# Kernel optimization log

Measured on AMD Instinct MI355X. Metric: run time of the kernel, lower is better.

Reference implementation:

```python
import jax, jax.numpy as jnp
import numpy as np

B, C, L = 4, 256, 4096
C8 = C // 8


def setup_inputs() -> dict:
    key = jax.random.key(0)
    ks = jax.random.split(key, 7)
    s = 0.05
    return {
        "x": jax.random.normal(ks[0], (B, C, L), dtype=jnp.float32),
        "Wq": jax.random.normal(ks[1], (C8, C), dtype=jnp.float32) * s,
        "bq": jax.random.normal(ks[2], (C8,), dtype=jnp.float32) * s,
        "Wk": jax.random.normal(ks[3], (C8, C), dtype=jnp.float32) * s,
        "bk": jax.random.normal(ks[4], (C8,), dtype=jnp.float32) * s,
        "Wv": jax.random.normal(ks[5], (C, C), dtype=jnp.float32) * s,
        "bv": jax.random.normal(ks[6], (C,), dtype=jnp.float32) * s,
        "gamma": jnp.zeros((1,), dtype=jnp.float32),
    }


def reference(x, Wq, bq, Wk, bk, Wv, bv, gamma):
    # 1x1 conv1d == pointwise linear over channel dim
    q = jnp.einsum("oc,bcl->bol", Wq, x) + bq[None, :, None]   # [B, C/8, L]
    k = jnp.einsum("oc,bcl->bol", Wk, x) + bk[None, :, None]   # [B, C/8, L]
    v = jnp.einsum("oc,bcl->bol", Wv, x) + bv[None, :, None]   # [B, C,   L]
    # scores[b, i, j] = q[:, i] . k[:, j]; softmax over j (unscaled, as in source)
    scores = jnp.einsum("bol,bom->blm", q, k)                  # [B, L, L]
    attn = jax.nn.softmax(scores, axis=-1)
    # out[b, c, i] = sum_j v[b, c, j] * attn[b, i, j]
    out = jnp.einsum("bcm,blm->bcl", v, attn)                  # [B, C, L]
    return gamma[0] * out + x
```

## Files before the change

kernel.cpp:

```cpp
#include <hip/hip_runtime.h>
#include <hip/hip_bf16.h>

#define B_   4
#define C_   256
#define L_   4096
#define CQ   32
#define PSTB 136

typedef __attribute__((ext_vector_type(8))) __bf16 bf16x8;
typedef __attribute__((ext_vector_type(4))) float  floatx4;
typedef __attribute__((ext_vector_type(2))) long long llx2;

static __device__ __forceinline__ unsigned short bits_of(float f) {
    __hip_bfloat16 h = __float2bfloat16(f);
    return *(unsigned short*)&h;
}

static __device__ __forceinline__ floatx4 mfma_fp8(long long a, long long b, floatx4 c) {
    return __builtin_amdgcn_mfma_f32_16x16x32_fp8_fp8(a, b, c, 0, 0, 0);
}

static __device__ __forceinline__ int vswz(int l) {
    return (l & ~63) | (((l >> 3) & 3) << 4) | (((l >> 5) & 1) << 3) | (l & 7);
}

__global__ __launch_bounds__(256) void wconvert_kernel(
    const float* __restrict__ Wq, const float* __restrict__ Wk,
    const float* __restrict__ Wv, __hip_bfloat16* __restrict__ Wb)
{
    int f = (blockIdx.x * 256 + threadIdx.x) * 4;
    int m = f >> 8, c = f & 255;
    const float* src;
    if (m < 32)      src = Wq + m * C_ + c;
    else if (m < 64) src = Wk + (m - 32) * C_ + c;
    else             src = Wv + (m - 64) * C_ + c;
    float4 v = *(const float4*)src;
    ushort4 o;
    o.x = bits_of(v.x); o.y = bits_of(v.y); o.z = bits_of(v.z); o.w = bits_of(v.w);
    *(ushort4*)(Wb + f) = o;
}

__global__ __launch_bounds__(512) void qkv_mfma_kernel(
    const float* __restrict__ x,
    const __hip_bfloat16* __restrict__ Wb,
    const float* __restrict__ bq, const float* __restrict__ bk,
    const float* __restrict__ bv,
    __hip_bfloat16* __restrict__ qT, __hip_bfloat16* __restrict__ kT,
    unsigned char* __restrict__ vO)
{
    __shared__ __hip_bfloat16 xsT[64 * 264];
    const int b  = blockIdx.x >> 6;
    const int l0 = (blockIdx.x & 63) << 6;
    const int t  = threadIdx.x;
    const float* xb = x + (size_t)b * C_ * L_;

    #pragma unroll
    for (int rep = 0; rep < 8; ++rep) {
        int c = rep * 32 + (t >> 4);
        float4 val = *(const float4*)(xb + (size_t)c * L_ + l0 + 4 * (t & 15));
        int r0 = 4 * (t & 15);
        xsT[(r0 + 0) * 264 + c] = __float2bfloat16(val.x);
        xsT[(r0 + 1) * 264 + c] = __float2bfloat16(val.y);
        xsT[(r0 + 2) * 264 + c] = __float2bfloat16(val.z);
        xsT[(r0 + 3) * 264 + c] = __float2bfloat16(val.w);
    }
    __syncthreads();

    const int w = t >> 6, lane = t & 63;
    const int lg = lane >> 4, lc = lane & 15;
    const int mtg0 = 5 * (w >> 1);
    const int lt0  = 2 * (w & 1);

    floatx4 acc[5][2];
    #pragma unroll
    for (int i = 0; i < 5; ++i) {
        int mtg = mtg0 + i;
        const float* bias; int o;
        if (mtg < 2)      { bias = bq; o = 16 * mtg; }
        else if (mtg < 4) { bias = bk; o = 16 * (mtg - 2); }
        else              { bias = bv; o = 16 * (mtg - 4); }
        float4 b4 = *(const float4*)(bias + o + 4 * lg);
        #pragma unroll
        for (int j = 0; j < 2; ++j) {
            acc[i][j][0] = b4.x; acc[i][j][1] = b4.y;
            acc[i][j][2] = b4.z; acc[i][j][3] = b4.w;
        }
    }

    #pragma unroll
    for (int ks = 0; ks < 8; ++ks) {
        bf16x8 a[5], bfr[2];
        #pragma unroll
        for (int i = 0; i < 5; ++i)
            a[i] = *(const bf16x8*)(Wb + (size_t)(16 * (mtg0 + i) + lc) * C_ + ks * 32 + 8 * lg);
        #pragma unroll
        for (int j = 0; j < 2; ++j)
            bfr[j] = *(const bf16x8*)(xsT + (16 * (lt0 + j) + lc) * 264 + ks * 32 + 8 * lg);
        #pragma unroll
        for (int i = 0; i < 5; ++i)
            #pragma unroll
            for (int j = 0; j < 2; ++j)
                acc[i][j] = __builtin_amdgcn_mfma_f32_16x16x32_bf16(a[i], bfr[j], acc[i][j], 0, 0, 0);
    }

    #pragma unroll
    for (int i = 0; i < 5; ++i) {
        int mtg = mtg0 + i;
        #pragma unroll
        for (int j = 0; j < 2; ++j) {
            int l = l0 + 16 * (lt0 + j) + lc;
            if (mtg < 4) {
                __hip_bfloat16* dst = (mtg < 2) ? qT : kT;
                int o = ((mtg < 2) ? 16 * mtg : 16 * (mtg - 2)) + 4 * lg;
                ushort4 pk;
                pk.x = bits_of(acc[i][j][0]); pk.y = bits_of(acc[i][j][1]);
                pk.z = bits_of(acc[i][j][2]); pk.w = bits_of(acc[i][j][3]);
                *(ushort4*)(dst + ((size_t)b * L_ + l) * CQ + o) = pk;
            } else {
                int c  = 16 * (mtg - 4) + 4 * lg;
                int ls = vswz(l);
                #pragma unroll
                for (int r = 0; r < 4; ++r) {
                    int pk = __builtin_amdgcn_cvt_pk_fp8_f32(acc[i][j][r], acc[i][j][r], 0, 0);
                    vO[((size_t)b * C_ + c + r) * L_ + ls] = (unsigned char)(pk & 0xFF);
                }
            }
        }
    }
}

__global__ __launch_bounds__(512, 2) void attn_kernel(
    const __hip_bfloat16* __restrict__ qT,
    const __hip_bfloat16* __restrict__ kT,
    const unsigned char* __restrict__ vI,
    const float* __restrict__ x,
    const float* __restrict__ gamma,
    float* __restrict__ out)
{
    __shared__ unsigned char p_lds[2][64 * PSTB];
    __shared__ float lsum_lds[64];

    const int b  = blockIdx.x >> 6;
    const int i0 = (blockIdx.x & 63) << 6;
    const int w    = threadIdx.x >> 6;
    const int lane = threadIdx.x & 63;
    const int lg = lane >> 4, lc = lane & 15;

    if (threadIdx.x < 64) lsum_lds[threadIdx.x] = 0.f;

    const __hip_bfloat16*  qTb = qT + (size_t)b * L_ * CQ;
    const __hip_bfloat16*  kTb = kT + (size_t)b * L_ * CQ;
    const unsigned char*   vb  = vI + (size_t)b * C_ * L_;

    bf16x8 qf[4];
    #pragma unroll
    for (int q2 = 0; q2 < 4; ++q2)
        qf[q2] = *(const bf16x8*)(qTb + (size_t)(i0 + 16 * q2 + lc) * CQ + 8 * lg);

    floatx4 vzero = 0.f;
    floatx4 acc[4][2];
    #pragma unroll
    for (int a = 0; a < 4; ++a)
        #pragma unroll
        for (int cc = 0; cc < 2; ++cc) acc[a][cc] = vzero;

    float lpart[4] = {0.f, 0.f, 0.f, 0.f};
    const float LOG2E = 1.44269504f;
    const float SH    = 14.4269504f;
    const float PCAP  = 440.f;

    bf16x8 kf = *(const bf16x8*)(kTb + (size_t)(16 * w + lc) * CQ + 8 * lg);

    for (int t = 0; t < 32; ++t) {
        const int j0  = t << 7;
        const int j0n = ((t + 1) & 31) << 7;
        unsigned char* pb = p_lds[t & 1];

        int4 vld[2][2];
        #pragma unroll
        for (int cti = 0; cti < 2; ++cti)
            #pragma unroll
            for (int g = 0; g < 2; ++g)
                vld[cti][g] = *(const int4*)(vb + (size_t)(32 * w + 16 * cti + lc) * L_
                                             + j0 + 64 * g + 16 * lg);
        bf16x8 nkf = *(const bf16x8*)(kTb + (size_t)(j0n + 16 * w + lc) * CQ + 8 * lg);

        #pragma unroll
        for (int q2 = 0; q2 < 4; ++q2) {
            floatx4 s = __builtin_amdgcn_mfma_f32_16x16x32_bf16(kf, qf[q2], vzero, 0, 0, 0);
            float p0 = fminf(exp2f(fmaf(s[0], LOG2E, -SH)), PCAP);
            float p1 = fminf(exp2f(fmaf(s[1], LOG2E, -SH)), PCAP);
            float p2 = fminf(exp2f(fmaf(s[2], LOG2E, -SH)), PCAP);
            float p3 = fminf(exp2f(fmaf(s[3], LOG2E, -SH)), PCAP);
            lpart[q2] += (p0 + p1) + (p2 + p3);
            int pk = __builtin_amdgcn_cvt_pk_fp8_f32(p0, p1, 0, 0);
            pk     = __builtin_amdgcn_cvt_pk_fp8_f32(p2, p3, pk, 1);
            *(unsigned int*)(pb + (16 * q2 + lc) * PSTB + 16 * w + 4 * lg) = (unsigned int)pk;
        }

        __syncthreads();

        #pragma unroll
        for (int kc = 0; kc < 4; ++kc) {
            long long pf[4];
            #pragma unroll
            for (int q2 = 0; q2 < 4; ++q2)
                pf[q2] = *(const long long*)(pb + (16 * q2 + lc) * PSTB + 32 * kc + 8 * lg);
            #pragma unroll
            for (int cti = 0; cti < 2; ++cti) {
                llx2 vv = __builtin_bit_cast(llx2, vld[cti][kc >> 1]);
                long long va = (kc & 1) ? vv[1] : vv[0];
                #pragma unroll
                for (int q2 = 0; q2 < 4; ++q2)
                    acc[q2][cti] = mfma_fp8(va, pf[q2], acc[q2][cti]);
            }
        }

        kf = nkf;
    }

    #pragma unroll
    for (int q2 = 0; q2 < 4; ++q2) {
        float lp = lpart[q2];
        lp += __shfl_xor(lp, 16);
        lp += __shfl_xor(lp, 32);
        if (lane < 16) atomicAdd(&lsum_lds[16 * q2 + lane], lp);
    }
    __syncthreads();

    const float g = gamma[0];
    const float* xb = x + (size_t)b * C_ * L_;
    float*       ob = out + (size_t)b * C_ * L_;
    #pragma unroll
    for (int q2 = 0; q2 < 4; ++q2) {
        float linv = 1.f / lsum_lds[16 * q2 + lc];
        #pragma unroll
        for (int cti = 0; cti < 2; ++cti) {
            #pragma unroll
            for (int r = 0; r < 4; ++r) {
                int c = 32 * w + 16 * cti + 4 * lg + r;
                size_t addr = (size_t)c * L_ + i0 + 16 * q2 + lc;
                ob[addr] = g * acc[q2][cti][r] * linv + xb[addr];
            }
        }
    }
}

extern "C" void kernel_launch(void* const* d_in, const int* in_sizes, int n_in,
                              void* d_out, int out_size, void* d_ws, size_t ws_size,
                              hipStream_t stream) {
    const float* x     = (const float*)d_in[0];
    const float* Wq    = (const float*)d_in[1];
    const float* bq    = (const float*)d_in[2];
    const float* Wk    = (const float*)d_in[3];
    const float* bk    = (const float*)d_in[4];
    const float* Wv    = (const float*)d_in[5];
    const float* bv    = (const float*)d_in[6];
    const float* gamma = (const float*)d_in[7];
    float* out = (float*)d_out;

    __hip_bfloat16* Wb = (__hip_bfloat16*)d_ws;
    __hip_bfloat16* qT = Wb + 320 * 256;
    __hip_bfloat16* kT = qT + (size_t)B_ * L_ * CQ;
    unsigned char*  v  = (unsigned char*)(kT + (size_t)B_ * L_ * CQ);

    wconvert_kernel<<<80, 256, 0, stream>>>(Wq, Wk, Wv, Wb);
    qkv_mfma_kernel<<<B_ * (L_ / 64), 512, 0, stream>>>(x, Wb, bq, bk, bv, qT, kT, v);
    attn_kernel<<<B_ * (L_ / 64), 512, 0, stream>>>(qT, kT, v, x, gamma, out);
}
```

Baseline: 74.63 us.

## Prefetch next V tile in attention, remap blocks, halve QKV tile size

The attention loop now loads the next iteration's V fragments one iteration ahead, alongside K, so global load latency overlaps with the current tile's MFMAs. The full __syncthreads is replaced by an explicit lgkmcnt wait plus s_barrier, and the PV MFMA phase runs at raised wave priority. Attention blocks are remapped so consecutive block IDs interleave batches, which changes how work spreads across XCDs and caches. The QKV projection kernel uses 32-column tiles, doubling its grid for more parallelism, at the cost of less weight reuse per block and more register pressure from the extra prefetch registers.

```diff
diff --git a/kernel.cpp b/kernel.cpp
--- a/kernel.cpp
+++ b/kernel.cpp
@@ -48,17 +48,17 @@
     __hip_bfloat16* __restrict__ qT, __hip_bfloat16* __restrict__ kT,
     unsigned char* __restrict__ vO)
 {
-    __shared__ __hip_bfloat16 xsT[64 * 264];
-    const int b  = blockIdx.x >> 6;
-    const int l0 = (blockIdx.x & 63) << 6;
+    __shared__ __hip_bfloat16 xsT[32 * 264];
+    const int b  = blockIdx.x >> 7;
+    const int l0 = (blockIdx.x & 127) << 5;
     const int t  = threadIdx.x;
     const float* xb = x + (size_t)b * C_ * L_;
 
     #pragma unroll
-    for (int rep = 0; rep < 8; ++rep) {
-        int c = rep * 32 + (t >> 4);
-        float4 val = *(const float4*)(xb + (size_t)c * L_ + l0 + 4 * (t & 15));
-        int r0 = 4 * (t & 15);
+    for (int rep = 0; rep < 4; ++rep) {
+        int c = rep * 64 + (t >> 3);
+        float4 val = *(const float4*)(xb + (size_t)c * L_ + l0 + 4 * (t & 7));
+        int r0 = 4 * (t & 7);
         xsT[(r0 + 0) * 264 + c] = __float2bfloat16(val.x);
         xsT[(r0 + 1) * 264 + c] = __float2bfloat16(val.y);
         xsT[(r0 + 2) * 264 + c] = __float2bfloat16(val.z);
@@ -69,9 +69,9 @@
     const int w = t >> 6, lane = t & 63;
     const int lg = lane >> 4, lc = lane & 15;
     const int mtg0 = 5 * (w >> 1);
-    const int lt0  = 2 * (w & 1);
-
-    floatx4 acc[5][2];
+    const int lt   = (w & 1);
+
+    floatx4 acc[5];
     #pragma unroll
     for (int i = 0; i < 5; ++i) {
         int mtg = mtg0 + i;
@@ -80,50 +80,39 @@
         else if (mtg < 4) { bias = bk; o = 16 * (mtg - 2); }
         else              { bias = bv; o = 16 * (mtg - 4); }
         float4 b4 = *(const float4*)(bias + o + 4 * lg);
-        #pragma unroll
-        for (int j = 0; j < 2; ++j) {
-            acc[i][j][0] = b4.x; acc[i][j][1] = b4.y;
-            acc[i][j][2] = b4.z; acc[i][j][3] = b4.w;
-        }
+        acc[i][0] = b4.x; acc[i][1] = b4.y; acc[i][2] = b4.z; acc[i][3] = b4.w;
     }
 
     #pragma unroll
     for (int ks = 0; ks < 8; ++ks) {
-        bf16x8 a[5], bfr[2];
+        bf16x8 a[5];
         #pragma unroll
         for (int i = 0; i < 5; ++i)
             a[i] = *(const bf16x8*)(Wb + (size_t)(16 * (mtg0 + i) + lc) * C_ + ks * 32 + 8 * lg);
-        #pragma unroll
-        for (int j = 0; j < 2; ++j)
-            bfr[j] = *(const bf16x8*)(xsT + (16 * (lt0 + j) + lc) * 264 + ks * 32 + 8 * lg);
+        bf16x8 bfr = *(const bf16x8*)(xsT + (16 * lt + lc) * 264 + ks * 32 + 8 * lg);
         #pragma unroll
         for (int i = 0; i < 5; ++i)
-            #pragma unroll
-            for (int j = 0; j < 2; ++j)
-                acc[i][j] = __builtin_amdgcn_mfma_f32_16x16x32_bf16(a[i], bfr[j], acc[i][j], 0, 0, 0);
-    }
-
+            acc[i] = __builtin_amdgcn_mfma_f32_16x16x32_bf16(a[i], bfr, acc[i], 0, 0, 0);
+    }
+
+    const int l = l0 + 16 * lt + lc;
     #pragma unroll
     for (int i = 0; i < 5; ++i) {
         int mtg = mtg0 + i;
-        #pragma unroll
-        for (int j = 0; j < 2; ++j) {
-            int l = l0 + 16 * (lt0 + j) + lc;
-            if (mtg < 4) {
-                __hip_bfloat16* dst = (mtg < 2) ? qT : kT;
-                int o = ((mtg < 2) ? 16 * mtg : 16 * (mtg - 2)) + 4 * lg;
-                ushort4 pk;
-                pk.x = bits_of(acc[i][j][0]); pk.y = bits_of(acc[i][j][1]);
-                pk.z = bits_of(acc[i][j][2]); pk.w = bits_of(acc[i][j][3]);
-                *(ushort4*)(dst + ((size_t)b * L_ + l) * CQ + o) = pk;
-            } else {
-                int c  = 16 * (mtg - 4) + 4 * lg;
-                int ls = vswz(l);
-                #pragma unroll
-                for (int r = 0; r < 4; ++r) {
-                    int pk = __builtin_amdgcn_cvt_pk_fp8_f32(acc[i][j][r], acc[i][j][r], 0, 0);
-                    vO[((size_t)b * C_ + c + r) * L_ + ls] = (unsigned char)(pk & 0xFF);
-                }
+        if (mtg < 4) {
+            __hip_bfloat16* dst = (mtg < 2) ? qT : kT;
+            int o = ((mtg < 2) ? 16 * mtg : 16 * (mtg - 2)) + 4 * lg;
+            ushort4 pk;
+            pk.x = bits_of(acc[i][0]); pk.y = bits_of(acc[i][1]);
+            pk.z = bits_of(acc[i][2]); pk.w = bits_of(acc[i][3]);
+            *(ushort4*)(dst + ((size_t)b * L_ + l) * CQ + o) = pk;
+        } else {
+            int c  = 16 * (mtg - 4) + 4 * lg;
+            int ls = vswz(l);
+            #pragma unroll
+            for (int r = 0; r < 4; ++r) {
+                int pk = __builtin_amdgcn_cvt_pk_fp8_f32(acc[i][r], acc[i][r], 0, 0);
+                vO[((size_t)b * C_ + c + r) * L_ + ls] = (unsigned char)(pk & 0xFF);
             }
         }
     }
@@ -140,8 +129,9 @@
     __shared__ unsigned char p_lds[2][64 * PSTB];
     __shared__ float lsum_lds[64];
 
-    const int b  = blockIdx.x >> 6;
-    const int i0 = (blockIdx.x & 63) << 6;
+    const int g  = blockIdx.x;
+    const int b  = (g & 7) >> 1;
+    const int i0 = ((((g >> 3) << 1) | (g & 1))) << 6;
     const int w    = threadIdx.x >> 6;
     const int lane = threadIdx.x & 63;
     const int lg = lane >> 4, lc = lane & 15;
@@ -169,21 +159,26 @@
     const float SH    = 14.4269504f;
     const float PCAP  = 440.f;
 
-    bf16x8 kf = *(const bf16x8*)(kTb + (size_t)(16 * w + lc) * CQ + 8 * lg);
+    const __hip_bfloat16* kp = kTb + (size_t)(16 * w + lc) * CQ + 8 * lg;
+    const unsigned char*  vp = vb + (size_t)(32 * w + lc) * L_ + 16 * lg;
+
+    bf16x8 kf  = *(const bf16x8*)kp;
+    int4 vc00 = *(const int4*)(vp);
+    int4 vc01 = *(const int4*)(vp + 64);
+    int4 vc10 = *(const int4*)(vp + 16 * L_);
+    int4 vc11 = *(const int4*)(vp + 16 * L_ + 64);
+
+    __syncthreads();
 
     for (int t = 0; t < 32; ++t) {
-        const int j0  = t << 7;
-        const int j0n = ((t + 1) & 31) << 7;
         unsigned char* pb = p_lds[t & 1];
-
-        int4 vld[2][2];
-        #pragma unroll
-        for (int cti = 0; cti < 2; ++cti)
-            #pragma unroll
-            for (int g = 0; g < 2; ++g)
-                vld[cti][g] = *(const int4*)(vb + (size_t)(32 * w + 16 * cti + lc) * L_
-                                             + j0 + 64 * g + 16 * lg);
-        bf16x8 nkf = *(const bf16x8*)(kTb + (size_t)(j0n + 16 * w + lc) * CQ + 8 * lg);
+        const int jn = ((t + 1) & 31) << 7;
+
+        bf16x8 kf_n = *(const bf16x8*)(kp + (size_t)jn * CQ);
+        int4 n00 = *(const int4*)(vp + jn);
+        int4 n01 = *(const int4*)(vp + jn + 64);
+        int4 n10 = *(const int4*)(vp + jn + 16 * L_);
+        int4 n11 = *(const int4*)(vp + jn + 16 * L_ + 64);
 
         #pragma unroll
         for (int q2 = 0; q2 < 4; ++q2) {
@@ -198,25 +193,31 @@
             *(unsigned int*)(pb + (16 * q2 + lc) * PSTB + 16 * w + 4 * lg) = (unsigned int)pk;
         }
 
-        __syncthreads();
-
+        asm volatile("s_waitcnt lgkmcnt(0)" ::: "memory");
+        __builtin_amdgcn_s_barrier();
+        __builtin_amdgcn_sched_barrier(0);
+
+        __builtin_amdgcn_s_setprio(1);
         #pragma unroll
         for (int kc = 0; kc < 4; ++kc) {
             long long pf[4];
             #pragma unroll
             for (int q2 = 0; q2 < 4; ++q2)
                 pf[q2] = *(const long long*)(pb + (16 * q2 + lc) * PSTB + 32 * kc + 8 * lg);
-            #pragma unroll
-            for (int cti = 0; cti < 2; ++cti) {
-                llx2 vv = __builtin_bit_cast(llx2, vld[cti][kc >> 1]);
-                long long va = (kc & 1) ? vv[1] : vv[0];
-                #pragma unroll
-                for (int q2 = 0; q2 < 4; ++q2)
-                    acc[q2][cti] = mfma_fp8(va, pf[q2], acc[q2][cti]);
+            llx2 v0 = __builtin_bit_cast(llx2, (kc >> 1) ? vc01 : vc00);
+            llx2 v1 = __builtin_bit_cast(llx2, (kc >> 1) ? vc11 : vc10);
+            long long va0 = (kc & 1) ? v0[1] : v0[0];
+            long long va1 = (kc & 1) ? v1[1] : v1[0];
+            #pragma unroll
+            for (int q2 = 0; q2 < 4; ++q2) {
+                acc[q2][0] = mfma_fp8(va0, pf[q2], acc[q2][0]);
+                acc[q2][1] = mfma_fp8(va1, pf[q2], acc[q2][1]);
             }
         }
-
-        kf = nkf;
+        __builtin_amdgcn_s_setprio(0);
+
+        kf = kf_n;
+        vc00 = n00; vc01 = n01; vc10 = n10; vc11 = n11;
     }
 
     #pragma unroll
@@ -228,7 +229,7 @@
     }
     __syncthreads();
 
-    const float g = gamma[0];
+    const float gm = gamma[0];
     const float* xb = x + (size_t)b * C_ * L_;
     float*       ob = out + (size_t)b * C_ * L_;
     #pragma unroll
@@ -240,7 +241,7 @@
             for (int r = 0; r < 4; ++r) {
                 int c = 32 * w + 16 * cti + 4 * lg + r;
                 size_t addr = (size_t)c * L_ + i0 + 16 * q2 + lc;
-                ob[addr] = g * acc[q2][cti][r] * linv + xb[addr];
+                ob[addr] = gm * acc[q2][cti][r] * linv + xb[addr];
             }
         }
     }
@@ -265,6 +266,6 @@
     unsigned char*  v  = (unsigned char*)(kT + (size_t)B_ * L_ * CQ);
 
     wconvert_kernel<<<80, 256, 0, stream>>>(Wq, Wk, Wv, Wb);
-    qkv_mfma_kernel<<<B_ * (L_ / 64), 512, 0, stream>>>(x, Wb, bq, bk, bv, qT, kT, v);
+    qkv_mfma_kernel<<<B_ * (L_ / 32), 512, 0, stream>>>(x, Wb, bq, bk, bv, qT, kT, v);
     attn_kernel<<<B_ * (L_ / 64), 512, 0, stream>>>(qT, kT, v, x, gamma, out);
 }
```

New measurement: 82.82 us. 1.11x slower.

## Software-pipeline P computation one tile ahead and remap block-to-batch ordering

Applied to the files above, without the earlier changes.

Restructures the attention main loop so the exp/fp8-packing of scores for tile t+1 is written to the alternate LDS buffer while the PV MFMAs for tile t run, with one barrier per iteration. K and V loads are prefetched one to two tiles ahead. The P layout in LDS is changed (new stride, permuted write offset) so each lane reads 32 contiguous bytes with two 16-byte loads. Blocks are also interleaved across batches, and exp2f is replaced by the hardware exp2 builtin. This adds register pressure from the extra prefetched tiles and relies on manual waitcnt and barrier placement being correct.

```diff
diff --git a/kernel.cpp b/kernel.cpp
--- a/kernel.cpp
+++ b/kernel.cpp
@@ -5,7 +5,7 @@
 #define C_   256
 #define L_   4096
 #define CQ   32
-#define PSTB 136
+#define PSTB 144
 
 typedef __attribute__((ext_vector_type(8))) __bf16 bf16x8;
 typedef __attribute__((ext_vector_type(4))) float  floatx4;
@@ -140,8 +140,9 @@
     __shared__ unsigned char p_lds[2][64 * PSTB];
     __shared__ float lsum_lds[64];
 
-    const int b  = blockIdx.x >> 6;
-    const int i0 = (blockIdx.x & 63) << 6;
+    const int g  = blockIdx.x;
+    const int b  = (g & 7) >> 1;
+    const int i0 = ((((g >> 3) << 1) | (g & 1))) << 6;
     const int w    = threadIdx.x >> 6;
     const int lane = threadIdx.x & 63;
     const int lg = lane >> 4, lc = lane & 15;
@@ -169,54 +170,86 @@
     const float SH    = 14.4269504f;
     const float PCAP  = 440.f;
 
-    bf16x8 kf = *(const bf16x8*)(kTb + (size_t)(16 * w + lc) * CQ + 8 * lg);
+    const __hip_bfloat16* kp = kTb + (size_t)(16 * w + lc) * CQ + 8 * lg;
+    const unsigned char*  vp = vb + (size_t)(32 * w + lc) * L_ + 16 * lg;
+    const int pwoff = 64 * (w & 1) + 32 * (lg >> 1) + 8 * (w >> 1) + 4 * (lg & 1);
+
+    bf16x8 kf0 = *(const bf16x8*)kp;
+    bf16x8 kA  = *(const bf16x8*)(kp + (size_t)(1 << 7) * CQ);
+    int4 vA0 = *(const int4*)(vp);
+    int4 vA1 = *(const int4*)(vp + 64);
+    int4 vA2 = *(const int4*)(vp + 16 * L_);
+    int4 vA3 = *(const int4*)(vp + 16 * L_ + 64);
+
+    #pragma unroll
+    for (int q2 = 0; q2 < 4; ++q2) {
+        floatx4 s = __builtin_amdgcn_mfma_f32_16x16x32_bf16(kf0, qf[q2], vzero, 0, 0, 0);
+        float p0 = fminf(__builtin_amdgcn_exp2f(fmaf(s[0], LOG2E, -SH)), PCAP);
+        float p1 = fminf(__builtin_amdgcn_exp2f(fmaf(s[1], LOG2E, -SH)), PCAP);
+        float p2 = fminf(__builtin_amdgcn_exp2f(fmaf(s[2], LOG2E, -SH)), PCAP);
+        float p3 = fminf(__builtin_amdgcn_exp2f(fmaf(s[3], LOG2E, -SH)), PCAP);
+        lpart[q2] += (p0 + p1) + (p2 + p3);
+        int pk = __builtin_amdgcn_cvt_pk_fp8_f32(p0, p1, 0, 0);
+        pk     = __builtin_amdgcn_cvt_pk_fp8_f32(p2, p3, pk, 1);
+        *(unsigned int*)(p_lds[0] + (16 * q2 + lc) * PSTB + pwoff) = (unsigned int)pk;
+    }
+    asm volatile("s_waitcnt lgkmcnt(0)" ::: "memory");
+    __builtin_amdgcn_s_barrier();
+    __builtin_amdgcn_sched_barrier(0);
 
     for (int t = 0; t < 32; ++t) {
-        const int j0  = t << 7;
-        const int j0n = ((t + 1) & 31) << 7;
-        unsigned char* pb = p_lds[t & 1];
-
-        int4 vld[2][2];
-        #pragma unroll
-        for (int cti = 0; cti < 2; ++cti)
-            #pragma unroll
-            for (int g = 0; g < 2; ++g)
-                vld[cti][g] = *(const int4*)(vb + (size_t)(32 * w + 16 * cti + lc) * L_
-                                             + j0 + 64 * g + 16 * lg);
-        bf16x8 nkf = *(const bf16x8*)(kTb + (size_t)(j0n + 16 * w + lc) * CQ + 8 * lg);
-
+        unsigned char* pbr = p_lds[t & 1];
+        unsigned char* pbw = p_lds[(t + 1) & 1];
+        const int jn1 = ((t + 1) & 31) << 7;
+        const int jn2 = ((t + 2) & 31) << 7;
+
+        bf16x8 kB = *(const bf16x8*)(kp + (size_t)jn2 * CQ);
+        int4 nV0 = *(const int4*)(vp + jn1);
+        int4 nV1 = *(const int4*)(vp + jn1 + 64);
+        int4 nV2 = *(const int4*)(vp + jn1 + 16 * L_);
+        int4 nV3 = *(const int4*)(vp + jn1 + 16 * L_ + 64);
+
+        int4 pr[4][2];
         #pragma unroll
         for (int q2 = 0; q2 < 4; ++q2) {
-            floatx4 s = __builtin_amdgcn_mfma_f32_16x16x32_bf16(kf, qf[q2], vzero, 0, 0, 0);
-            float p0 = fminf(exp2f(fmaf(s[0], LOG2E, -SH)), PCAP);
-            float p1 = fminf(exp2f(fmaf(s[1], LOG2E, -SH)), PCAP);
-            float p2 = fminf(exp2f(fmaf(s[2], LOG2E, -SH)), PCAP);
-            float p3 = fminf(exp2f(fmaf(s[3], LOG2E, -SH)), PCAP);
+            pr[q2][0] = *(const int4*)(pbr + (16 * q2 + lc) * PSTB + lg * 32);
+            pr[q2][1] = *(const int4*)(pbr + (16 * q2 + lc) * PSTB + lg * 32 + 16);
+        }
+
+        #pragma unroll
+        for (int q2 = 0; q2 < 4; ++q2) {
+            floatx4 s = __builtin_amdgcn_mfma_f32_16x16x32_bf16(kA, qf[q2], vzero, 0, 0, 0);
+            float p0 = fminf(__builtin_amdgcn_exp2f(fmaf(s[0], LOG2E, -SH)), PCAP);
+            float p1 = fminf(__builtin_amdgcn_exp2f(fmaf(s[1], LOG2E, -SH)), PCAP);
+            float p2 = fminf(__builtin_amdgcn_exp2f(fmaf(s[2], LOG2E, -SH)), PCAP);
+            float p3 = fminf(__builtin_amdgcn_exp2f(fmaf(s[3], LOG2E, -SH)), PCAP);
             lpart[q2] += (p0 + p1) + (p2 + p3);
             int pk = __builtin_amdgcn_cvt_pk_fp8_f32(p0, p1, 0, 0);
             pk     = __builtin_amdgcn_cvt_pk_fp8_f32(p2, p3, pk, 1);
-            *(unsigned int*)(pb + (16 * q2 + lc) * PSTB + 16 * w + 4 * lg) = (unsigned int)pk;
-        }
-
-        __syncthreads();
-
-        #pragma unroll
-        for (int kc = 0; kc < 4; ++kc) {
-            long long pf[4];
+            *(unsigned int*)(pbw + (16 * q2 + lc) * PSTB + pwoff) = (unsigned int)pk;
+        }
+
+        #pragma unroll
+        for (int h = 0; h < 2; ++h) {
+            llx2 v0 = __builtin_bit_cast(llx2, h ? vA1 : vA0);
+            llx2 v1 = __builtin_bit_cast(llx2, h ? vA3 : vA2);
             #pragma unroll
-            for (int q2 = 0; q2 < 4; ++q2)
-                pf[q2] = *(const long long*)(pb + (16 * q2 + lc) * PSTB + 32 * kc + 8 * lg);
-            #pragma unroll
-            for (int cti = 0; cti < 2; ++cti) {
-                llx2 vv = __builtin_bit_cast(llx2, vld[cti][kc >> 1]);
-                long long va = (kc & 1) ? vv[1] : vv[0];
+            for (int kk = 0; kk < 2; ++kk) {
                 #pragma unroll
-                for (int q2 = 0; q2 < 4; ++q2)
-                    acc[q2][cti] = mfma_fp8(va, pf[q2], acc[q2][cti]);
+                for (int q2 = 0; q2 < 4; ++q2) {
+                    llx2 pp = __builtin_bit_cast(llx2, pr[q2][h]);
+                    acc[q2][0] = mfma_fp8(v0[kk], pp[kk], acc[q2][0]);
+                    acc[q2][1] = mfma_fp8(v1[kk], pp[kk], acc[q2][1]);
+                }
             }
         }
 
-        kf = nkf;
+        asm volatile("s_waitcnt lgkmcnt(0)" ::: "memory");
+        __builtin_amdgcn_s_barrier();
+        __builtin_amdgcn_sched_barrier(0);
+
+        kA = kB;
+        vA0 = nV0; vA1 = nV1; vA2 = nV2; vA3 = nV3;
     }
 
     #pragma unroll
@@ -228,7 +261,7 @@
     }
     __syncthreads();
 
-    const float g = gamma[0];
+    const float gm = gamma[0];
     const float* xb = x + (size_t)b * C_ * L_;
     float*       ob = out + (size_t)b * C_ * L_;
     #pragma unroll
@@ -240,7 +273,7 @@
             for (int r = 0; r < 4; ++r) {
                 int c = 32 * w + 16 * cti + 4 * lg + r;
                 size_t addr = (size_t)c * L_ + i0 + 16 * q2 + lc;
-                ob[addr] = g * acc[q2][cti][r] * linv + xb[addr];
+                ob[addr] = gm * acc[q2][cti][r] * linv + xb[addr];
             }
         }
     }
```

New measurement: 69.54 us, median of 2. 6.8% less time.
